# Kernel optimization log

Measured on AMD Instinct MI355X. Metric: run time of the kernel, lower is better.

## Reference

```python
import jax, jax.numpy as jnp
import numpy as np

B, T, P, H, K = 64, 110, 64, 256, 16


def _gru_scan(x_seq, h0, Wih, Whh, bih, bhh):
    """PyTorch-convention GRU. x_seq: (B,L,D), h0: (B,H). Returns (outs (B,L,H), h_last (B,H))."""
    def step(h, x_t):
        gi = x_t @ Wih.T + bih          # (B, 3H)
        gh = h @ Whh.T + bhh            # (B, 3H)
        i_r, i_z, i_n = jnp.split(gi, 3, axis=-1)
        h_r, h_z, h_n = jnp.split(gh, 3, axis=-1)
        r = jax.nn.sigmoid(i_r + h_r)
        zg = jax.nn.sigmoid(i_z + h_z)
        n = jnp.tanh(i_n + r * h_n)
        h_new = (1.0 - zg) * n + zg * h
        return h_new, h_new
    h_last, outs = jax.lax.scan(step, h0, jnp.swapaxes(x_seq, 0, 1))
    return jnp.swapaxes(outs, 0, 1), h_last


def setup_inputs() -> dict:
    key = jax.random.key(0)
    ks = jax.random.split(key, 24)
    s = 0.05
    n = lambda k, shape: (jax.random.normal(k, shape, jnp.float32) * s)
    X = jax.random.normal(ks[0], (B, T, P), jnp.float32)
    # connection: 16 distinct nonzero rows per column, sorted (mimics np.where on a binary mask)
    r = jax.random.uniform(ks[1], (P, P))
    conn_idx = jnp.sort(jnp.argsort(r, axis=0)[:K].T, axis=1).astype(jnp.int32)  # (P, K)
    return dict(
        X=X, conn_idx=conn_idx,
        W_ih_left=n(ks[2], (3 * H, P)), W_hh_left=n(ks[3], (3 * H, H)),
        b_ih_left=n(ks[4], (3 * H,)), b_hh_left=n(ks[5], (3 * H,)),
        W_ih_1=n(ks[6], (3 * H, H)), W_hh_1=n(ks[7], (3 * H, H)),
        b_ih_1=n(ks[8], (3 * H,)), b_hh_1=n(ks[9], (3 * H,)),
        W_mu=n(ks[10], (H, H)), b_mu=n(ks[11], (H,)),
        W_std=n(ks[12], (H, H)), b_std=n(ks[13], (H,)),
        W_mean=n(ks[14], (P, H)), b_mean=n(ks[15], (P,)),
        W_disp=n(ks[16], (P, H)), b_disp=n(ks[17], (P,)),
        W_ih_nets=n(ks[18], (P, 3 * H, K)), W_hh_nets=n(ks[19], (P, 3 * H, H)),
        b_ih_nets=n(ks[20], (P, 3 * H)), b_hh_nets=n(ks[21], (P, 3 * H)),
        W_lin=n(ks[22], (P, 1, H)), b_lin=n(ks[23], (P, 1)),
        z_noise=jax.random.normal(jax.random.fold_in(key, 123), (B, H), jnp.float32),
    )


def reference(X, conn_idx, W_ih_left, W_hh_left, b_ih_left, b_hh_left,
              W_ih_1, W_hh_1, b_ih_1, b_hh_1,
              W_mu, b_mu, W_std, b_std, W_mean, b_mean, W_disp, b_disp,
              W_ih_nets, W_hh_nets, b_ih_nets, b_hh_nets, W_lin, b_lin, z_noise):
    Bb, Tt, Pp = X.shape
    Hh = W_hh_left.shape[1]
    # phase=0, mode='train': prepend a zero timestep
    X_pad = jnp.concatenate([jnp.zeros((Bb, 1, Pp), X.dtype), X], axis=1)  # (B, T+1, P)

    # encoder: gru_left over first 10 real timesteps, h0 = 0
    h0 = jnp.zeros((Bb, Hh), X.dtype)
    _, h_left = _gru_scan(X_pad[:, 1:11, :], h0, W_ih_left, W_hh_left, b_ih_left, b_hh_left)
    # gru_1: single recurrent step with input h_left, hidden 0
    _, h1 = _gru_scan(h_left[:, None, :], h0, W_ih_1, W_hh_1, b_ih_1, b_hh_1)  # (B, H)

    mu = h1 @ W_mu.T + b_mu
    log_var = h1 @ W_std.T + b_std
    mean_ = jnp.clip(jnp.exp(h1 @ W_mean.T + b_mean), 1e-5, 1e6)          # MeanAct
    disp_ = jnp.clip(jax.nn.softplus(h1 @ W_disp.T + b_disp), 1e-4, 1e4)  # DispAct
    z = mu + jnp.exp(0.5 * log_var) * z_noise                             # reparameterize

    # per-series connectivity gather: (B, T+1, P, K) -> (P, B, T+1, K)
    Xg = jnp.transpose(X_pad[:, :, conn_idx], (2, 0, 1, 3))
    # GRU input: cat(X[:, 0:1, :], X[:, 11:-1, :]) -> length L = T - 10
    seq = jnp.concatenate([Xg[:, :, 0:1, :], Xg[:, :, 11:-1, :]], axis=2)  # (P, B, L, K)

    h0_nets = jnp.broadcast_to(z, (Pp, Bb, Hh))
    outs, _ = jax.vmap(_gru_scan, in_axes=(0, 0, 0, 0, 0, 0))(
        seq, h0_nets, W_ih_nets, W_hh_nets, b_ih_nets, b_hh_nets)  # (P, B, L, H)
    outs = jax.nn.relu(outs)
    pred = jnp.einsum('pblh,poh->pblo', outs, W_lin) + b_lin[:, None, None, :]  # (P, B, L, 1)

    return pred, log_var, mu, mean_, disp_
```

## Files before the change

### kernel.cpp

```cpp
#include <hip/hip_runtime.h>


#define OFF_LV   409600
#define OFF_MU   425984
#define OFF_MEAN 442368
#define OFF_DISP 446464

typedef __attribute__((ext_vector_type(8))) short  bf16x8;
typedef __attribute__((ext_vector_type(4))) float  f32x4;

__device__ __forceinline__ float bf2f(unsigned short u) {
    union { unsigned int i; float f; } v; v.i = ((unsigned int)u) << 16; return v.f;
}
__device__ __forceinline__ unsigned short f2bf(float f) {
    union { float f; unsigned int i; } v; v.f = f;
    unsigned int x = v.i;
    return (unsigned short)((x + 0x7FFFu + ((x >> 16) & 1u)) >> 16);
}
__device__ __forceinline__ unsigned short f2bf_fast(float f) {
    return (unsigned short)((__float_as_uint(f) + 0x8000u) >> 16);
}
__device__ __forceinline__ bf16x8 pack8(const float* pf) {
    union { unsigned int u[4]; bf16x8 v; } r;
    const float4 a = *(const float4*)pf;
    const float4 b = *(const float4*)(pf + 4);
    r.u[0] = ((__float_as_uint(a.x) + 0x8000u) >> 16) | ((__float_as_uint(a.y) + 0x8000u) & 0xFFFF0000u);
    r.u[1] = ((__float_as_uint(a.z) + 0x8000u) >> 16) | ((__float_as_uint(a.w) + 0x8000u) & 0xFFFF0000u);
    r.u[2] = ((__float_as_uint(b.x) + 0x8000u) >> 16) | ((__float_as_uint(b.y) + 0x8000u) & 0xFFFF0000u);
    r.u[3] = ((__float_as_uint(b.z) + 0x8000u) >> 16) | ((__float_as_uint(b.w) + 0x8000u) & 0xFFFF0000u);
    return r.v;
}
__device__ __forceinline__ float sigm(float x) {
    return __builtin_amdgcn_rcpf(1.0f + __expf(-x));
}
__device__ __forceinline__ float tanh_fast(float x) {
    return 2.0f * __builtin_amdgcn_rcpf(1.0f + __expf(-2.0f * x)) - 1.0f;
}

#define MFMA(a, b, c) __builtin_amdgcn_mfma_f32_16x16x32_bf16((a), (b), (c), 0, 0, 0)

__global__ __launch_bounds__(512, 1) void encoder_mfma(
    const float* __restrict__ X,
    const float* __restrict__ Wihl_f, const float* __restrict__ Whhl_f,
    const float* __restrict__ bihl,   const float* __restrict__ bhhl,
    const float* __restrict__ Wih1_f, const float* __restrict__ bih1,
    const float* __restrict__ bhh1,
    const float* __restrict__ Wmu_f,  const float* __restrict__ bmu,
    const float* __restrict__ Wstd_f, const float* __restrict__ bstd,
    const float* __restrict__ Wmean_f,const float* __restrict__ bmean,
    const float* __restrict__ Wdisp_f,const float* __restrict__ bdisp,
    float* __restrict__ out)
{
    const int b0   = blockIdx.x * 16;
    const int tid  = threadIdx.x;
    const int wave = tid >> 6;
    const int lane = tid & 63;
    const int quad = lane >> 4;
    const int ncol = lane & 15;
    const int j0   = wave * 32 + ncol;
    const int j1   = j0 + 16;

    __shared__ __align__(16) unsigned short hs[2][16][264];
    __shared__ __align__(16) unsigned short xs[2][16][72];
    __shared__ __align__(16) unsigned short wihl_s[768][72];
    __shared__ float bR[256], bZ[256], bIN[256], bHN[256];
    __shared__ float b1R[256], b1Z[256], b1IN[256], b1HN[256];

    for (int i = tid; i < 768 * 64; i += 512) {
        int row = i >> 6, col = i & 63;
        wihl_s[row][col] = f2bf_fast(Wihl_f[i]);
    }
    for (int i = tid; i < 256; i += 512) {
        bR[i]   = bihl[i]       + bhhl[i];
        bZ[i]   = bihl[256 + i] + bhhl[256 + i];
        bIN[i]  = bihl[512 + i];
        bHN[i]  = bhhl[512 + i];
        b1R[i]  = bih1[i]       + bhh1[i];
        b1Z[i]  = bih1[256 + i] + bhh1[256 + i];
        b1IN[i] = bih1[512 + i];
        b1HN[i] = bhh1[512 + i];
    }
    for (int i = tid; i < 16 * 264; i += 512)
        (&hs[0][0][0])[i] = 0;
    for (int i = tid; i < 1024; i += 512) {
        int b = i >> 6, f = i & 63;
        xs[0][b][f] = f2bf_fast(X[((b0 + b) * 110 + 0) * 64 + f]);
    }

    bf16x8 w_r[2][8], w_z[2][8], w_n[2][8];
    #pragma unroll
    for (int s = 0; s < 2; s++) {
        const int j = s ? j1 : j0;
        #pragma unroll
        for (int k0 = 0; k0 < 8; k0++) {
            const int ko = k0 * 32 + quad * 8;
            w_r[s][k0] = pack8(Whhl_f + (size_t)(j)       * 256 + ko);
            w_z[s][k0] = pack8(Whhl_f + (size_t)(256 + j) * 256 + ko);
            w_n[s][k0] = pack8(Whhl_f + (size_t)(512 + j) * 256 + ko);
        }
    }

    float hreg[2][4];
    #pragma unroll
    for (int s = 0; s < 2; s++)
        #pragma unroll
        for (int r = 0; r < 4; r++) hreg[s][r] = 0.f;

    __syncthreads();

    for (int t = 0; t < 10; t++) {
        const int cur = t & 1, nxt = cur ^ 1;
        f32x4 acc_r[2]  = {{0,0,0,0},{0,0,0,0}};
        f32x4 acc_z[2]  = {{0,0,0,0},{0,0,0,0}};
        f32x4 acc_in[2] = {{0,0,0,0},{0,0,0,0}};
        f32x4 acc_hn[2] = {{0,0,0,0},{0,0,0,0}};

        #pragma unroll
        for (int ks = 0; ks < 2; ks++) {
            const int ko = ks * 32 + quad * 8;
            bf16x8 a = *(const bf16x8*)&xs[cur][ncol][ko];
            #pragma unroll
            for (int s = 0; s < 2; s++) {
                const int j = s ? j1 : j0;
                bf16x8 br = *(const bf16x8*)&wihl_s[j][ko];
                bf16x8 bz = *(const bf16x8*)&wihl_s[256 + j][ko];
                bf16x8 bn = *(const bf16x8*)&wihl_s[512 + j][ko];
                acc_r[s]  = MFMA(a, br, acc_r[s]);
                acc_z[s]  = MFMA(a, bz, acc_z[s]);
                acc_in[s] = MFMA(a, bn, acc_in[s]);
            }
        }
        #pragma unroll
        for (int ks = 0; ks < 8; ks++) {
            bf16x8 a = *(const bf16x8*)&hs[cur][ncol][ks * 32 + quad * 8];
            #pragma unroll
            for (int s = 0; s < 2; s++) {
                acc_r[s]  = MFMA(a, w_r[s][ks], acc_r[s]);
                acc_z[s]  = MFMA(a, w_z[s][ks], acc_z[s]);
                acc_hn[s] = MFMA(a, w_n[s][ks], acc_hn[s]);
            }
        }
        #pragma unroll
        for (int s = 0; s < 2; s++) {
            const int j = s ? j1 : j0;
            #pragma unroll
            for (int r = 0; r < 4; r++) {
                float rg = sigm(acc_r[s][r] + bR[j]);
                float zg = sigm(acc_z[s][r] + bZ[j]);
                float nn = tanh_fast(acc_in[s][r] + bIN[j] + rg * (acc_hn[s][r] + bHN[j]));
                float hv = (1.f - zg) * nn + zg * hreg[s][r];
                hreg[s][r] = hv;
                hs[nxt][quad * 4 + r][j] = f2bf(hv);
            }
        }
        if (t < 9)
            for (int i = tid; i < 1024; i += 512) {
                int b = i >> 6, f = i & 63;
                xs[nxt][b][f] = f2bf_fast(X[((b0 + b) * 110 + (t + 1)) * 64 + f]);
            }
        __syncthreads();
    }

    {
        f32x4 acc_r[2]  = {{0,0,0,0},{0,0,0,0}};
        f32x4 acc_z[2]  = {{0,0,0,0},{0,0,0,0}};
        f32x4 acc_in[2] = {{0,0,0,0},{0,0,0,0}};
        #pragma unroll 2
        for (int ks = 0; ks < 8; ks++) {
            const int ko = ks * 32 + quad * 8;
            bf16x8 a = *(const bf16x8*)&hs[0][ncol][ko];
            #pragma unroll
            for (int s = 0; s < 2; s++) {
                const int j = s ? j1 : j0;
                bf16x8 br = pack8(Wih1_f + (size_t)(j)       * 256 + ko);
                bf16x8 bz = pack8(Wih1_f + (size_t)(256 + j) * 256 + ko);
                bf16x8 bn = pack8(Wih1_f + (size_t)(512 + j) * 256 + ko);
                acc_r[s]  = MFMA(a, br, acc_r[s]);
                acc_z[s]  = MFMA(a, bz, acc_z[s]);
                acc_in[s] = MFMA(a, bn, acc_in[s]);
            }
        }
        #pragma unroll
        for (int s = 0; s < 2; s++) {
            const int j = s ? j1 : j0;
            #pragma unroll
            for (int r = 0; r < 4; r++) {
                float rg = sigm(acc_r[s][r] + b1R[j]);
                float zg = sigm(acc_z[s][r] + b1Z[j]);
                float nn = tanh_fast(acc_in[s][r] + b1IN[j] + rg * b1HN[j]);
                float hv = (1.f - zg) * nn;
                hs[1][quad * 4 + r][j] = f2bf(hv);
            }
        }
        __syncthreads();
    }

    {
        f32x4 acc_mu[2] = {{0,0,0,0},{0,0,0,0}};
        f32x4 acc_lv[2] = {{0,0,0,0},{0,0,0,0}};
        f32x4 acc_md[2] = {{0,0,0,0},{0,0,0,0}};
        const bool do_mean = (wave < 2), do_disp = (wave >= 2 && wave < 4);
        const int jm0 = (wave & 1) * 32 + ncol, jm1 = jm0 + 16;

        #pragma unroll 2
        for (int ks = 0; ks < 8; ks++) {
            const int ko = ks * 32 + quad * 8;
            bf16x8 a = *(const bf16x8*)&hs[1][ncol][ko];
            #pragma unroll
            for (int s = 0; s < 2; s++) {
                const int j = s ? j1 : j0;
                bf16x8 bmu8 = pack8(Wmu_f  + (size_t)j * 256 + ko);
                bf16x8 blv8 = pack8(Wstd_f + (size_t)j * 256 + ko);
                acc_mu[s] = MFMA(a, bmu8, acc_mu[s]);
                acc_lv[s] = MFMA(a, blv8, acc_lv[s]);
                if (do_mean || do_disp) {
                    const int jm = s ? jm1 : jm0;
                    bf16x8 md8 = do_mean ? pack8(Wmean_f + (size_t)jm * 256 + ko)
                                         : pack8(Wdisp_f + (size_t)jm * 256 + ko);
                    acc_md[s] = MFMA(a, md8, acc_md[s]);
                }
            }
        }
        #pragma unroll
        for (int s = 0; s < 2; s++) {
            const int j = s ? j1 : j0;
            const float bmu_v = bmu[j], blv_v = bstd[j];
            #pragma unroll
            for (int r = 0; r < 4; r++) {
                int b = b0 + quad * 4 + r;
                out[OFF_MU + b * 256 + j] = acc_mu[s][r] + bmu_v;
                out[OFF_LV + b * 256 + j] = acc_lv[s][r] + blv_v;
            }
        }
        if (do_mean) {
            #pragma unroll
            for (int s = 0; s < 2; s++) {
                const int jm = s ? jm1 : jm0;
                const float bm = bmean[jm];
                #pragma unroll
                for (int r = 0; r < 4; r++) {
                    int b = b0 + quad * 4 + r;
                    out[OFF_MEAN + b * 64 + jm] =
                        fminf(fmaxf(__expf(acc_md[s][r] + bm), 1e-5f), 1e6f);
                }
            }
        } else if (do_disp) {
            #pragma unroll
            for (int s = 0; s < 2; s++) {
                const int jm = s ? jm1 : jm0;
                const float bd = bdisp[jm];
                #pragma unroll
                for (int r = 0; r < 4; r++) {
                    int b = b0 + quad * 4 + r;
                    float v = acc_md[s][r] + bd;
                    float sp = (v > 20.f) ? v : log1pf(__expf(v));
                    out[OFF_DISP + b * 64 + jm] = fminf(fmaxf(sp, 1e-4f), 1e4f);
                }
            }
        }
    }
}

__global__ __launch_bounds__(512, 2) void nets_kernel(
    const float* __restrict__ X,
    const int*   __restrict__ conn,
    const float* __restrict__ Wih,
    const float* __restrict__ Whh_f,
    const float* __restrict__ bih,
    const float* __restrict__ bhh,
    const float* __restrict__ Wlin,
    const float* __restrict__ blin,
    const float* __restrict__ znoise,
    float*       __restrict__ out)
{
    const int p    = blockIdx.x;
    const int b0   = blockIdx.y * 16;
    const int tid  = threadIdx.x;
    const int wave = tid >> 6;
    const int lane = tid & 63;
    const int quad = lane >> 4;
    const int ncol = lane & 15;
    const int j0   = wave * 32 + ncol;
    const int j1   = j0 + 16;

    __shared__ __align__(16) unsigned short hs[2][16][264];
    __shared__ __align__(16) unsigned short xs[2][16][16];
    __shared__ __align__(16) unsigned short wih_s[768][16];
    __shared__ float bR[256], bZ[256], bIN[256], bHN[256], wlin_s[256];
    __shared__ float predw[2][8][16];
    __shared__ int   conn_s[16];

    for (int i = tid; i < 768 * 16; i += 512)
        (&wih_s[0][0])[i] = f2bf_fast(Wih[p * 768 * 16 + i]);
    for (int i = tid; i < 256; i += 512) {
        bR[i]  = bih[p * 768 + i]       + bhh[p * 768 + i];
        bZ[i]  = bih[p * 768 + 256 + i] + bhh[p * 768 + 256 + i];
        bIN[i] = bih[p * 768 + 512 + i];
        bHN[i] = bhh[p * 768 + 512 + i];
        wlin_s[i] = Wlin[p * 256 + i];
    }
    if (tid < 16) conn_s[tid] = conn[p * 16 + tid];

    for (int i = tid; i < 16 * 264; i += 512) {
        int bb = i / 264, jj = i - bb * 264;
        unsigned short v = 0;
        if (jj < 256) {
            int gi = (b0 + bb) * 256 + jj;
            v = f2bf(out[OFF_MU + gi] + __expf(0.5f * out[OFF_LV + gi]) * znoise[gi]);
        }
        hs[0][bb][jj] = v;
    }
    if (tid < 256) xs[0][tid >> 4][tid & 15] = 0;

    float hreg[2][4];
    #pragma unroll
    for (int s = 0; s < 2; s++)
        #pragma unroll
        for (int r = 0; r < 4; r++) {
            int gi = (b0 + quad * 4 + r) * 256 + (s ? j1 : j0);
            hreg[s][r] = out[OFF_MU + gi] + __expf(0.5f * out[OFF_LV + gi]) * znoise[gi];
        }

    const size_t whh_off = (size_t)p * 768 * 256;
    bf16x8 w_r[2][8], w_z[2][8], w_n[2][8];
    #pragma unroll
    for (int s = 0; s < 2; s++) {
        const int j = s ? j1 : j0;
        #pragma unroll
        for (int k0 = 0; k0 < 8; k0++) {
            const int ko = k0 * 32 + quad * 8;
            w_r[s][k0] = pack8(Whh_f + whh_off + (size_t)(j)       * 256 + ko);
            w_z[s][k0] = pack8(Whh_f + whh_off + (size_t)(256 + j) * 256 + ko);
            w_n[s][k0] = pack8(Whh_f + whh_off + (size_t)(512 + j) * 256 + ko);
        }
    }

    __syncthreads();

    const float blin_v = blin[p];
    const bf16x8 ZERO8 = {0, 0, 0, 0, 0, 0, 0, 0};

    for (int t = 0; t < 100; t++) {
        const int cur = t & 1, nxt = cur ^ 1;
        f32x4 acc_r[2]  = {{0,0,0,0},{0,0,0,0}};
        f32x4 acc_z[2]  = {{0,0,0,0},{0,0,0,0}};
        f32x4 acc_in[2] = {{0,0,0,0},{0,0,0,0}};
        f32x4 acc_hn[2] = {{0,0,0,0},{0,0,0,0}};

        {
            bf16x8 a, br0, bz0, bn0, br1, bz1, bn1;
            if (quad < 2) {
                a   = *(const bf16x8*)&xs[cur][ncol][quad * 8];
                br0 = *(const bf16x8*)&wih_s[j0][quad * 8];
                bz0 = *(const bf16x8*)&wih_s[256 + j0][quad * 8];
                bn0 = *(const bf16x8*)&wih_s[512 + j0][quad * 8];
                br1 = *(const bf16x8*)&wih_s[j1][quad * 8];
                bz1 = *(const bf16x8*)&wih_s[256 + j1][quad * 8];
                bn1 = *(const bf16x8*)&wih_s[512 + j1][quad * 8];
            } else {
                a = ZERO8; br0 = bz0 = bn0 = br1 = bz1 = bn1 = ZERO8;
            }
            acc_r[0]  = MFMA(a, br0, acc_r[0]);  acc_r[1]  = MFMA(a, br1, acc_r[1]);
            acc_z[0]  = MFMA(a, bz0, acc_z[0]);  acc_z[1]  = MFMA(a, bz1, acc_z[1]);
            acc_in[0] = MFMA(a, bn0, acc_in[0]); acc_in[1] = MFMA(a, bn1, acc_in[1]);
        }
        #pragma unroll
        for (int k0 = 0; k0 < 8; k0++) {
            bf16x8 a = *(const bf16x8*)&hs[cur][ncol][k0 * 32 + quad * 8];
            acc_r[0]  = MFMA(a, w_r[0][k0], acc_r[0]);
            acc_r[1]  = MFMA(a, w_r[1][k0], acc_r[1]);
            acc_z[0]  = MFMA(a, w_z[0][k0], acc_z[0]);
            acc_z[1]  = MFMA(a, w_z[1][k0], acc_z[1]);
            acc_hn[0] = MFMA(a, w_n[0][k0], acc_hn[0]);
            acc_hn[1] = MFMA(a, w_n[1][k0], acc_hn[1]);
        }

        float pv[4] = {0.f, 0.f, 0.f, 0.f};
        #pragma unroll
        for (int s = 0; s < 2; s++) {
            const int j = s ? j1 : j0;
            const float b_r = bR[j], b_z = bZ[j], b_in = bIN[j], b_hn = bHN[j];
            const float wl = wlin_s[j];
            #pragma unroll
            for (int r = 0; r < 4; r++) {
                float rg = sigm(acc_r[s][r] + b_r);
                float zg = sigm(acc_z[s][r] + b_z);
                float nn = tanh_fast(acc_in[s][r] + b_in + rg * (acc_hn[s][r] + b_hn));
                float hv = (1.f - zg) * nn + zg * hreg[s][r];
                hreg[s][r] = hv;
                pv[r] += fmaxf(hv, 0.f) * wl;
            }
        }
        #pragma unroll
        for (int r = 0; r < 4; r++) {
            float v = pv[r];
            v += __shfl_xor(v, 1, 64);
            v += __shfl_xor(v, 2, 64);
            v += __shfl_xor(v, 4, 64);
            v += __shfl_xor(v, 8, 64);
            pv[r] = v;
        }

        #pragma unroll
        for (int r = 0; r < 4; r++) {
            hs[nxt][quad * 4 + r][j0] = f2bf_fast(hreg[0][r]);
            hs[nxt][quad * 4 + r][j1] = f2bf_fast(hreg[1][r]);
        }
        if (ncol == 0) {
            #pragma unroll
            for (int r = 0; r < 4; r++)
                predw[cur][wave][quad * 4 + r] = pv[r];
        }
        if (tid < 256) {
            int gb = tid >> 4, gk = tid & 15;
            unsigned short v = 0;
            if (t < 99) v = f2bf_fast(X[(size_t)((b0 + gb) * 110 + (10 + t)) * 64 + conn_s[gk]]);
            xs[nxt][gb][gk] = v;
        }

        __syncthreads();

        if (tid < 16) {
            float s = blin_v;
            #pragma unroll
            for (int w = 0; w < 8; w++) s += predw[cur][w][tid];
            out[(size_t)(p * 64 + b0 + tid) * 100 + t] = s;
        }
    }
}

extern "C" void kernel_launch(void* const* d_in, const int* in_sizes, int n_in,
                              void* d_out, int out_size, void* d_ws, size_t ws_size,
                              hipStream_t stream) {
    const float* X      = (const float*)d_in[0];
    const int*   conn   = (const int*)d_in[1];
    const float* Wihl   = (const float*)d_in[2];
    const float* Whhl   = (const float*)d_in[3];
    const float* bihl   = (const float*)d_in[4];
    const float* bhhl   = (const float*)d_in[5];
    const float* Wih1   = (const float*)d_in[6];
    const float* bih1   = (const float*)d_in[8];
    const float* bhh1   = (const float*)d_in[9];
    const float* Wmu    = (const float*)d_in[10];
    const float* bmu    = (const float*)d_in[11];
    const float* Wstd   = (const float*)d_in[12];
    const float* bstd   = (const float*)d_in[13];
    const float* Wmean  = (const float*)d_in[14];
    const float* bmean  = (const float*)d_in[15];
    const float* Wdisp  = (const float*)d_in[16];
    const float* bdisp  = (const float*)d_in[17];
    const float* Wihn   = (const float*)d_in[18];
    const float* Whhn   = (const float*)d_in[19];
    const float* bihn   = (const float*)d_in[20];
    const float* bhhn   = (const float*)d_in[21];
    const float* Wlin   = (const float*)d_in[22];
    const float* blin   = (const float*)d_in[23];
    const float* znoise = (const float*)d_in[24];

    float* out = (float*)d_out;
    (void)d_ws; (void)ws_size;

    encoder_mfma<<<4, 512, 0, stream>>>(
        X, Wihl, Whhl, bihl, bhhl, Wih1, bih1, bhh1,
        Wmu, bmu, Wstd, bstd, Wmean, bmean, Wdisp, bdisp, out);

    nets_kernel<<<dim3(64, 4), 512, 0, stream>>>(
        X, conn, Wihn, Whhn, bihn, bhhn, Wlin, blin, znoise, out);
}
```

Before: 528.6 us.

## Fuse encoder GRU into per-series nets kernel, recomputing encoder redundantly per block

Merges the two launches into one kernel. Each of the 256 blocks recomputes the 10-step encoder GRU, the gru_1 step and the mu/logvar heads for its 16-sample batch slice. The block then seeds its per-series GRU directly from the reparameterized z kept in registers and LDS, instead of reading mu and log_var back from global memory. This removes the second kernel launch and the serial dependency on a 4-block encoder kernel, at the cost of 64x redundant encoder work. The encoder input weights are now read from global memory (cache) rather than staged in LDS, to keep shared memory small enough for two blocks per CU.

```diff
diff --git a/kernel.cpp b/kernel.cpp
--- a/kernel.cpp
+++ b/kernel.cpp
@@ -39,8 +39,9 @@
 
 #define MFMA(a, b, c) __builtin_amdgcn_mfma_f32_16x16x32_bf16((a), (b), (c), 0, 0, 0)
 
-__global__ __launch_bounds__(512, 1) void encoder_mfma(
+__global__ __launch_bounds__(512, 2) void granger_fused(
     const float* __restrict__ X,
+    const int*   __restrict__ conn,
     const float* __restrict__ Wihl_f, const float* __restrict__ Whhl_f,
     const float* __restrict__ bihl,   const float* __restrict__ bhhl,
     const float* __restrict__ Wih1_f, const float* __restrict__ bih1,
@@ -49,227 +50,9 @@
     const float* __restrict__ Wstd_f, const float* __restrict__ bstd,
     const float* __restrict__ Wmean_f,const float* __restrict__ bmean,
     const float* __restrict__ Wdisp_f,const float* __restrict__ bdisp,
-    float* __restrict__ out)
-{
-    const int b0   = blockIdx.x * 16;
-    const int tid  = threadIdx.x;
-    const int wave = tid >> 6;
-    const int lane = tid & 63;
-    const int quad = lane >> 4;
-    const int ncol = lane & 15;
-    const int j0   = wave * 32 + ncol;
-    const int j1   = j0 + 16;
-
-    __shared__ __align__(16) unsigned short hs[2][16][264];
-    __shared__ __align__(16) unsigned short xs[2][16][72];
-    __shared__ __align__(16) unsigned short wihl_s[768][72];
-    __shared__ float bR[256], bZ[256], bIN[256], bHN[256];
-    __shared__ float b1R[256], b1Z[256], b1IN[256], b1HN[256];
-
-    for (int i = tid; i < 768 * 64; i += 512) {
-        int row = i >> 6, col = i & 63;
-        wihl_s[row][col] = f2bf_fast(Wihl_f[i]);
-    }
-    for (int i = tid; i < 256; i += 512) {
-        bR[i]   = bihl[i]       + bhhl[i];
-        bZ[i]   = bihl[256 + i] + bhhl[256 + i];
-        bIN[i]  = bihl[512 + i];
-        bHN[i]  = bhhl[512 + i];
-        b1R[i]  = bih1[i]       + bhh1[i];
-        b1Z[i]  = bih1[256 + i] + bhh1[256 + i];
-        b1IN[i] = bih1[512 + i];
-        b1HN[i] = bhh1[512 + i];
-    }
-    for (int i = tid; i < 16 * 264; i += 512)
-        (&hs[0][0][0])[i] = 0;
-    for (int i = tid; i < 1024; i += 512) {
-        int b = i >> 6, f = i & 63;
-        xs[0][b][f] = f2bf_fast(X[((b0 + b) * 110 + 0) * 64 + f]);
-    }
-
-    bf16x8 w_r[2][8], w_z[2][8], w_n[2][8];
-    #pragma unroll
-    for (int s = 0; s < 2; s++) {
-        const int j = s ? j1 : j0;
-        #pragma unroll
-        for (int k0 = 0; k0 < 8; k0++) {
-            const int ko = k0 * 32 + quad * 8;
-            w_r[s][k0] = pack8(Whhl_f + (size_t)(j)       * 256 + ko);
-            w_z[s][k0] = pack8(Whhl_f + (size_t)(256 + j) * 256 + ko);
-            w_n[s][k0] = pack8(Whhl_f + (size_t)(512 + j) * 256 + ko);
-        }
-    }
-
-    float hreg[2][4];
-    #pragma unroll
-    for (int s = 0; s < 2; s++)
-        #pragma unroll
-        for (int r = 0; r < 4; r++) hreg[s][r] = 0.f;
-
-    __syncthreads();
-
-    for (int t = 0; t < 10; t++) {
-        const int cur = t & 1, nxt = cur ^ 1;
-        f32x4 acc_r[2]  = {{0,0,0,0},{0,0,0,0}};
-        f32x4 acc_z[2]  = {{0,0,0,0},{0,0,0,0}};
-        f32x4 acc_in[2] = {{0,0,0,0},{0,0,0,0}};
-        f32x4 acc_hn[2] = {{0,0,0,0},{0,0,0,0}};
-
-        #pragma unroll
-        for (int ks = 0; ks < 2; ks++) {
-            const int ko = ks * 32 + quad * 8;
-            bf16x8 a = *(const bf16x8*)&xs[cur][ncol][ko];
-            #pragma unroll
-            for (int s = 0; s < 2; s++) {
-                const int j = s ? j1 : j0;
-                bf16x8 br = *(const bf16x8*)&wihl_s[j][ko];
-                bf16x8 bz = *(const bf16x8*)&wihl_s[256 + j][ko];
-                bf16x8 bn = *(const bf16x8*)&wihl_s[512 + j][ko];
-                acc_r[s]  = MFMA(a, br, acc_r[s]);
-                acc_z[s]  = MFMA(a, bz, acc_z[s]);
-                acc_in[s] = MFMA(a, bn, acc_in[s]);
-            }
-        }
-        #pragma unroll
-        for (int ks = 0; ks < 8; ks++) {
-            bf16x8 a = *(const bf16x8*)&hs[cur][ncol][ks * 32 + quad * 8];
-            #pragma unroll
-            for (int s = 0; s < 2; s++) {
-                acc_r[s]  = MFMA(a, w_r[s][ks], acc_r[s]);
-                acc_z[s]  = MFMA(a, w_z[s][ks], acc_z[s]);
-                acc_hn[s] = MFMA(a, w_n[s][ks], acc_hn[s]);
-            }
-        }
-        #pragma unroll
-        for (int s = 0; s < 2; s++) {
-            const int j = s ? j1 : j0;
-            #pragma unroll
-            for (int r = 0; r < 4; r++) {
-                float rg = sigm(acc_r[s][r] + bR[j]);
-                float zg = sigm(acc_z[s][r] + bZ[j]);
-                float nn = tanh_fast(acc_in[s][r] + bIN[j] + rg * (acc_hn[s][r] + bHN[j]));
-                float hv = (1.f - zg) * nn + zg * hreg[s][r];
-                hreg[s][r] = hv;
-                hs[nxt][quad * 4 + r][j] = f2bf(hv);
-            }
-        }
-        if (t < 9)
-            for (int i = tid; i < 1024; i += 512) {
-                int b = i >> 6, f = i & 63;
-                xs[nxt][b][f] = f2bf_fast(X[((b0 + b) * 110 + (t + 1)) * 64 + f]);
-            }
-        __syncthreads();
-    }
-
-    {
-        f32x4 acc_r[2]  = {{0,0,0,0},{0,0,0,0}};
-        f32x4 acc_z[2]  = {{0,0,0,0},{0,0,0,0}};
-        f32x4 acc_in[2] = {{0,0,0,0},{0,0,0,0}};
-        #pragma unroll 2
-        for (int ks = 0; ks < 8; ks++) {
-            const int ko = ks * 32 + quad * 8;
-            bf16x8 a = *(const bf16x8*)&hs[0][ncol][ko];
-            #pragma unroll
-            for (int s = 0; s < 2; s++) {
-                const int j = s ? j1 : j0;
-                bf16x8 br = pack8(Wih1_f + (size_t)(j)       * 256 + ko);
-                bf16x8 bz = pack8(Wih1_f + (size_t)(256 + j) * 256 + ko);
-                bf16x8 bn = pack8(Wih1_f + (size_t)(512 + j) * 256 + ko);
-                acc_r[s]  = MFMA(a, br, acc_r[s]);
-                acc_z[s]  = MFMA(a, bz, acc_z[s]);
-                acc_in[s] = MFMA(a, bn, acc_in[s]);
-            }
-        }
-        #pragma unroll
-        for (int s = 0; s < 2; s++) {
-            const int j = s ? j1 : j0;
-            #pragma unroll
-            for (int r = 0; r < 4; r++) {
-                float rg = sigm(acc_r[s][r] + b1R[j]);
-                float zg = sigm(acc_z[s][r] + b1Z[j]);
-                float nn = tanh_fast(acc_in[s][r] + b1IN[j] + rg * b1HN[j]);
-                float hv = (1.f - zg) * nn;
-                hs[1][quad * 4 + r][j] = f2bf(hv);
-            }
-        }
-        __syncthreads();
-    }
-
-    {
-        f32x4 acc_mu[2] = {{0,0,0,0},{0,0,0,0}};
-        f32x4 acc_lv[2] = {{0,0,0,0},{0,0,0,0}};
-        f32x4 acc_md[2] = {{0,0,0,0},{0,0,0,0}};
-        const bool do_mean = (wave < 2), do_disp = (wave >= 2 && wave < 4);
-        const int jm0 = (wave & 1) * 32 + ncol, jm1 = jm0 + 16;
-
-        #pragma unroll 2
-        for (int ks = 0; ks < 8; ks++) {
-            const int ko = ks * 32 + quad * 8;
-            bf16x8 a = *(const bf16x8*)&hs[1][ncol][ko];
-            #pragma unroll
-            for (int s = 0; s < 2; s++) {
-                const int j = s ? j1 : j0;
-                bf16x8 bmu8 = pack8(Wmu_f  + (size_t)j * 256 + ko);
-                bf16x8 blv8 = pack8(Wstd_f + (size_t)j * 256 + ko);
-                acc_mu[s] = MFMA(a, bmu8, acc_mu[s]);
-                acc_lv[s] = MFMA(a, blv8, acc_lv[s]);
-                if (do_mean || do_disp) {
-                    const int jm = s ? jm1 : jm0;
-                    bf16x8 md8 = do_mean ? pack8(Wmean_f + (size_t)jm * 256 + ko)
-                                         : pack8(Wdisp_f + (size_t)jm * 256 + ko);
-                    acc_md[s] = MFMA(a, md8, acc_md[s]);
-                }
-            }
-        }
-        #pragma unroll
-        for (int s = 0; s < 2; s++) {
-            const int j = s ? j1 : j0;
-            const float bmu_v = bmu[j], blv_v = bstd[j];
-            #pragma unroll
-            for (int r = 0; r < 4; r++) {
-                int b = b0 + quad * 4 + r;
-                out[OFF_MU + b * 256 + j] = acc_mu[s][r] + bmu_v;
-                out[OFF_LV + b * 256 + j] = acc_lv[s][r] + blv_v;
-            }
-        }
-        if (do_mean) {
-            #pragma unroll
-            for (int s = 0; s < 2; s++) {
-                const int jm = s ? jm1 : jm0;
-                const float bm = bmean[jm];
-                #pragma unroll
-                for (int r = 0; r < 4; r++) {
-                    int b = b0 + quad * 4 + r;
-                    out[OFF_MEAN + b * 64 + jm] =
-                        fminf(fmaxf(__expf(acc_md[s][r] + bm), 1e-5f), 1e6f);
-                }
-            }
-        } else if (do_disp) {
-            #pragma unroll
-            for (int s = 0; s < 2; s++) {
-                const int jm = s ? jm1 : jm0;
-                const float bd = bdisp[jm];
-                #pragma unroll
-                for (int r = 0; r < 4; r++) {
-                    int b = b0 + quad * 4 + r;
-                    float v = acc_md[s][r] + bd;
-                    float sp = (v > 20.f) ? v : log1pf(__expf(v));
-                    out[OFF_DISP + b * 64 + jm] = fminf(fmaxf(sp, 1e-4f), 1e4f);
-                }
-            }
-        }
-    }
-}
-
-__global__ __launch_bounds__(512, 2) void nets_kernel(
-    const float* __restrict__ X,
-    const int*   __restrict__ conn,
-    const float* __restrict__ Wih,
-    const float* __restrict__ Whh_f,
-    const float* __restrict__ bih,
-    const float* __restrict__ bhh,
-    const float* __restrict__ Wlin,
-    const float* __restrict__ blin,
+    const float* __restrict__ Wih,    const float* __restrict__ Whh_f,
+    const float* __restrict__ bih,    const float* __restrict__ bhh,
+    const float* __restrict__ Wlin,   const float* __restrict__ blin,
     const float* __restrict__ znoise,
     float*       __restrict__ out)
 {
@@ -284,11 +67,216 @@
     const int j1   = j0 + 16;
 
     __shared__ __align__(16) unsigned short hs[2][16][264];
-    __shared__ __align__(16) unsigned short xs[2][16][16];
+    __shared__ __align__(16) unsigned short xse[2][16][72];
+    __shared__ __align__(16) unsigned short xsn[2][16][16];
     __shared__ __align__(16) unsigned short wih_s[768][16];
-    __shared__ float bR[256], bZ[256], bIN[256], bHN[256], wlin_s[256];
+    __shared__ float bR[256], bZ[256], bIN[256], bHN[256];
+    __shared__ float b1R[256], b1Z[256], b1IN[256], b1HN[256];
+    __shared__ float wlin_s[256];
     __shared__ float predw[2][8][16];
     __shared__ int   conn_s[16];
+
+    for (int i = tid; i < 256; i += 512) {
+        bR[i]   = bihl[i]       + bhhl[i];
+        bZ[i]   = bihl[256 + i] + bhhl[256 + i];
+        bIN[i]  = bihl[512 + i];
+        bHN[i]  = bhhl[512 + i];
+        b1R[i]  = bih1[i]       + bhh1[i];
+        b1Z[i]  = bih1[256 + i] + bhh1[256 + i];
+        b1IN[i] = bih1[512 + i];
+        b1HN[i] = bhh1[512 + i];
+    }
+    for (int i = tid; i < 16 * 264; i += 512)
+        (&hs[0][0][0])[i] = 0;
+    for (int i = tid; i < 1024; i += 512) {
+        int b = i >> 6, f = i & 63;
+        xse[0][b][f] = f2bf_fast(X[((b0 + b) * 110 + 0) * 64 + f]);
+    }
+
+    bf16x8 w_r[2][8], w_z[2][8], w_n[2][8];
+    #pragma unroll
+    for (int s = 0; s < 2; s++) {
+        const int j = s ? j1 : j0;
+        #pragma unroll
+        for (int k0 = 0; k0 < 8; k0++) {
+            const int ko = k0 * 32 + quad * 8;
+            w_r[s][k0] = pack8(Whhl_f + (size_t)(j)       * 256 + ko);
+            w_z[s][k0] = pack8(Whhl_f + (size_t)(256 + j) * 256 + ko);
+            w_n[s][k0] = pack8(Whhl_f + (size_t)(512 + j) * 256 + ko);
+        }
+    }
+
+    float hreg[2][4];
+    #pragma unroll
+    for (int s = 0; s < 2; s++)
+        #pragma unroll
+        for (int r = 0; r < 4; r++) hreg[s][r] = 0.f;
+
+    __syncthreads();
+
+    const float* wxl = Wihl_f;
+    for (int t = 0; t < 10; t++) {
+        asm("" : "+v"(wxl));
+        const int cur = t & 1, nxt = cur ^ 1;
+        f32x4 acc_r[2]  = {{0,0,0,0},{0,0,0,0}};
+        f32x4 acc_z[2]  = {{0,0,0,0},{0,0,0,0}};
+        f32x4 acc_in[2] = {{0,0,0,0},{0,0,0,0}};
+        f32x4 acc_hn[2] = {{0,0,0,0},{0,0,0,0}};
+
+        #pragma unroll
+        for (int ks = 0; ks < 2; ks++) {
+            const int ko = ks * 32 + quad * 8;
+            bf16x8 a = *(const bf16x8*)&xse[cur][ncol][ko];
+            #pragma unroll
+            for (int s = 0; s < 2; s++) {
+                const int j = s ? j1 : j0;
+                bf16x8 br = pack8(wxl + (size_t)(j)       * 64 + ko);
+                bf16x8 bz = pack8(wxl + (size_t)(256 + j) * 64 + ko);
+                bf16x8 bn = pack8(wxl + (size_t)(512 + j) * 64 + ko);
+                acc_r[s]  = MFMA(a, br, acc_r[s]);
+                acc_z[s]  = MFMA(a, bz, acc_z[s]);
+                acc_in[s] = MFMA(a, bn, acc_in[s]);
+            }
+        }
+        #pragma unroll
+        for (int ks = 0; ks < 8; ks++) {
+            bf16x8 a = *(const bf16x8*)&hs[cur][ncol][ks * 32 + quad * 8];
+            #pragma unroll
+            for (int s = 0; s < 2; s++) {
+                acc_r[s]  = MFMA(a, w_r[s][ks], acc_r[s]);
+                acc_z[s]  = MFMA(a, w_z[s][ks], acc_z[s]);
+                acc_hn[s] = MFMA(a, w_n[s][ks], acc_hn[s]);
+            }
+        }
+        #pragma unroll
+        for (int s = 0; s < 2; s++) {
+            const int j = s ? j1 : j0;
+            #pragma unroll
+            for (int r = 0; r < 4; r++) {
+                float rg = sigm(acc_r[s][r] + bR[j]);
+                float zg = sigm(acc_z[s][r] + bZ[j]);
+                float nn = tanh_fast(acc_in[s][r] + bIN[j] + rg * (acc_hn[s][r] + bHN[j]));
+                float hv = (1.f - zg) * nn + zg * hreg[s][r];
+                hreg[s][r] = hv;
+                hs[nxt][quad * 4 + r][j] = f2bf(hv);
+            }
+        }
+        if (t < 9)
+            for (int i = tid; i < 1024; i += 512) {
+                int b = i >> 6, f = i & 63;
+                xse[nxt][b][f] = f2bf_fast(X[((b0 + b) * 110 + (t + 1)) * 64 + f]);
+            }
+        __syncthreads();
+    }
+
+    {
+        f32x4 acc_r[2]  = {{0,0,0,0},{0,0,0,0}};
+        f32x4 acc_z[2]  = {{0,0,0,0},{0,0,0,0}};
+        f32x4 acc_in[2] = {{0,0,0,0},{0,0,0,0}};
+        #pragma unroll 2
+        for (int ks = 0; ks < 8; ks++) {
+            const int ko = ks * 32 + quad * 8;
+            bf16x8 a = *(const bf16x8*)&hs[0][ncol][ko];
+            #pragma unroll
+            for (int s = 0; s < 2; s++) {
+                const int j = s ? j1 : j0;
+                bf16x8 br = pack8(Wih1_f + (size_t)(j)       * 256 + ko);
+                bf16x8 bz = pack8(Wih1_f + (size_t)(256 + j) * 256 + ko);
+                bf16x8 bn = pack8(Wih1_f + (size_t)(512 + j) * 256 + ko);
+                acc_r[s]  = MFMA(a, br, acc_r[s]);
+                acc_z[s]  = MFMA(a, bz, acc_z[s]);
+                acc_in[s] = MFMA(a, bn, acc_in[s]);
+            }
+        }
+        #pragma unroll
+        for (int s = 0; s < 2; s++) {
+            const int j = s ? j1 : j0;
+            #pragma unroll
+            for (int r = 0; r < 4; r++) {
+                float rg = sigm(acc_r[s][r] + b1R[j]);
+                float zg = sigm(acc_z[s][r] + b1Z[j]);
+                float nn = tanh_fast(acc_in[s][r] + b1IN[j] + rg * b1HN[j]);
+                float hv = (1.f - zg) * nn;
+                hs[1][quad * 4 + r][j] = f2bf(hv);
+            }
+        }
+        __syncthreads();
+    }
+
+    {
+        f32x4 acc_mu[2] = {{0,0,0,0},{0,0,0,0}};
+        f32x4 acc_lv[2] = {{0,0,0,0},{0,0,0,0}};
+        f32x4 acc_md[2] = {{0,0,0,0},{0,0,0,0}};
+        const bool headp   = (p == 0);
+        const bool do_mean = headp && (wave < 2);
+        const bool do_disp = headp && (wave >= 2 && wave < 4);
+        const int jm0 = (wave & 1) * 32 + ncol, jm1 = jm0 + 16;
+
+        #pragma unroll 2
+        for (int ks = 0; ks < 8; ks++) {
+            const int ko = ks * 32 + quad * 8;
+            bf16x8 a = *(const bf16x8*)&hs[1][ncol][ko];
+            #pragma unroll
+            for (int s = 0; s < 2; s++) {
+                const int j = s ? j1 : j0;
+                bf16x8 bmu8 = pack8(Wmu_f  + (size_t)j * 256 + ko);
+                bf16x8 blv8 = pack8(Wstd_f + (size_t)j * 256 + ko);
+                acc_mu[s] = MFMA(a, bmu8, acc_mu[s]);
+                acc_lv[s] = MFMA(a, blv8, acc_lv[s]);
+                if (do_mean || do_disp) {
+                    const int jm = s ? jm1 : jm0;
+                    bf16x8 md8 = do_mean ? pack8(Wmean_f + (size_t)jm * 256 + ko)
+                                         : pack8(Wdisp_f + (size_t)jm * 256 + ko);
+                    acc_md[s] = MFMA(a, md8, acc_md[s]);
+                }
+            }
+        }
+        #pragma unroll
+        for (int s = 0; s < 2; s++) {
+            const int j = s ? j1 : j0;
+            const float bmu_v = bmu[j], blv_v = bstd[j];
+            #pragma unroll
+            for (int r = 0; r < 4; r++) {
+                const int row = quad * 4 + r, b = b0 + row;
+                float muv = acc_mu[s][r] + bmu_v;
+                float lvv = acc_lv[s][r] + blv_v;
+                if (headp) {
+                    out[OFF_MU + b * 256 + j] = muv;
+                    out[OFF_LV + b * 256 + j] = lvv;
+                }
+                float zv = muv + __expf(0.5f * lvv) * znoise[b * 256 + j];
+                hreg[s][r] = zv;
+                hs[0][row][j] = f2bf(zv);
+            }
+        }
+        if (do_mean) {
+            #pragma unroll
+            for (int s = 0; s < 2; s++) {
+                const int jm = s ? jm1 : jm0;
+                const float bm = bmean[jm];
+                #pragma unroll
+                for (int r = 0; r < 4; r++) {
+                    int b = b0 + quad * 4 + r;
+                    out[OFF_MEAN + b * 64 + jm] =
+                        fminf(fmaxf(__expf(acc_md[s][r] + bm), 1e-5f), 1e6f);
+                }
+            }
+        } else if (do_disp) {
+            #pragma unroll
+            for (int s = 0; s < 2; s++) {
+                const int jm = s ? jm1 : jm0;
+                const float bd = bdisp[jm];
+                #pragma unroll
+                for (int r = 0; r < 4; r++) {
+                    int b = b0 + quad * 4 + r;
+                    float v = acc_md[s][r] + bd;
+                    float sp = (v > 20.f) ? v : log1pf(__expf(v));
+                    out[OFF_DISP + b * 64 + jm] = fminf(fmaxf(sp, 1e-4f), 1e4f);
+                }
+            }
+        }
+    }
+    __syncthreads();
 
     for (int i = tid; i < 768 * 16; i += 512)
         (&wih_s[0][0])[i] = f2bf_fast(Wih[p * 768 * 16 + i]);
@@ -300,29 +288,9 @@
         wlin_s[i] = Wlin[p * 256 + i];
     }
     if (tid < 16) conn_s[tid] = conn[p * 16 + tid];
-
-    for (int i = tid; i < 16 * 264; i += 512) {
-        int bb = i / 264, jj = i - bb * 264;
-        unsigned short v = 0;
-        if (jj < 256) {
-            int gi = (b0 + bb) * 256 + jj;
-            v = f2bf(out[OFF_MU + gi] + __expf(0.5f * out[OFF_LV + gi]) * znoise[gi]);
-        }
-        hs[0][bb][jj] = v;
-    }
-    if (tid < 256) xs[0][tid >> 4][tid & 15] = 0;
-
-    float hreg[2][4];
-    #pragma unroll
-    for (int s = 0; s < 2; s++)
-        #pragma unroll
-        for (int r = 0; r < 4; r++) {
-            int gi = (b0 + quad * 4 + r) * 256 + (s ? j1 : j0);
-            hreg[s][r] = out[OFF_MU + gi] + __expf(0.5f * out[OFF_LV + gi]) * znoise[gi];
-        }
+    if (tid < 256) xsn[0][tid >> 4][tid & 15] = 0;
 
     const size_t whh_off = (size_t)p * 768 * 256;
-    bf16x8 w_r[2][8], w_z[2][8], w_n[2][8];
     #pragma unroll
     for (int s = 0; s < 2; s++) {
         const int j = s ? j1 : j0;
@@ -350,7 +318,7 @@
         {
             bf16x8 a, br0, bz0, bn0, br1, bz1, bn1;
             if (quad < 2) {
-                a   = *(const bf16x8*)&xs[cur][ncol][quad * 8];
+                a   = *(const bf16x8*)&xsn[cur][ncol][quad * 8];
                 br0 = *(const bf16x8*)&wih_s[j0][quad * 8];
                 bz0 = *(const bf16x8*)&wih_s[256 + j0][quad * 8];
                 bn0 = *(const bf16x8*)&wih_s[512 + j0][quad * 8];
@@ -415,7 +383,7 @@
             int gb = tid >> 4, gk = tid & 15;
             unsigned short v = 0;
             if (t < 99) v = f2bf_fast(X[(size_t)((b0 + gb) * 110 + (10 + t)) * 64 + conn_s[gk]]);
-            xs[nxt][gb][gk] = v;
+            xsn[nxt][gb][gk] = v;
         }
 
         __syncthreads();
@@ -460,10 +428,8 @@
     float* out = (float*)d_out;
     (void)d_ws; (void)ws_size;
 
-    encoder_mfma<<<4, 512, 0, stream>>>(
-        X, Wihl, Whhl, bihl, bhhl, Wih1, bih1, bhh1,
-        Wmu, bmu, Wstd, bstd, Wmean, bmean, Wdisp, bdisp, out);
-
-    nets_kernel<<<dim3(64, 4), 512, 0, stream>>>(
-        X, conn, Wihn, Whhn, bihn, bhhn, Wlin, blin, znoise, out);
-}
+    granger_fused<<<dim3(64, 4), 512, 0, stream>>>(
+        X, conn, Wihl, Whhl, bihl, bhhl, Wih1, bih1, bhh1,
+        Wmu, bmu, Wstd, bstd, Wmean, bmean, Wdisp, bdisp,
+        Wihn, Whhn, bihn, bhhn, Wlin, blin, znoise, out);
+}
```

New measurement: 582.4 us. 10.2% more time.

## Move latent heads from encoder into nets kernel with redundant per-block recompute

Applied to the files above, without the earlier changes.

The encoder kernel now stops after the GRU and writes h1 as bf16 to workspace. The mu/log_var/mean/disp projections and the reparameterization move into the nets kernel: every block recomputes mu and log_var for its 16 batch rows and seeds its hidden state directly. Only the p==0 blocks write the head outputs. This takes the head GEMMs off the 4-block encoder's serial path, at the cost of each of the 256 nets blocks re-reading the Wmu/Wstd weights and doing redundant MFMA work.

```diff
diff --git a/kernel.cpp b/kernel.cpp
--- a/kernel.cpp
+++ b/kernel.cpp
@@ -39,17 +39,13 @@
 
 #define MFMA(a, b, c) __builtin_amdgcn_mfma_f32_16x16x32_bf16((a), (b), (c), 0, 0, 0)
 
-__global__ __launch_bounds__(512, 1) void encoder_mfma(
+__global__ __launch_bounds__(512, 1) void encoder_core(
     const float* __restrict__ X,
     const float* __restrict__ Wihl_f, const float* __restrict__ Whhl_f,
     const float* __restrict__ bihl,   const float* __restrict__ bhhl,
     const float* __restrict__ Wih1_f, const float* __restrict__ bih1,
     const float* __restrict__ bhh1,
-    const float* __restrict__ Wmu_f,  const float* __restrict__ bmu,
-    const float* __restrict__ Wstd_f, const float* __restrict__ bstd,
-    const float* __restrict__ Wmean_f,const float* __restrict__ bmean,
-    const float* __restrict__ Wdisp_f,const float* __restrict__ bdisp,
-    float* __restrict__ out)
+    unsigned short* __restrict__ h1out)
 {
     const int b0   = blockIdx.x * 16;
     const int tid  = threadIdx.x;
@@ -195,17 +191,73 @@
         __syncthreads();
     }
 
+    for (int i = tid; i < 16 * 256; i += 512) {
+        int row = i >> 8, j = i & 255;
+        h1out[(size_t)(b0 + row) * 256 + j] = hs[1][row][j];
+    }
+}
+
+__global__ __launch_bounds__(512, 2) void nets_kernel(
+    const float* __restrict__ X,
+    const int*   __restrict__ conn,
+    const float* __restrict__ Wih,
+    const float* __restrict__ Whh_f,
+    const float* __restrict__ bih,
+    const float* __restrict__ bhh,
+    const float* __restrict__ Wlin,
+    const float* __restrict__ blin,
+    const float* __restrict__ znoise,
+    const unsigned short* __restrict__ h1g,
+    const float* __restrict__ Wmu_f,  const float* __restrict__ bmu,
+    const float* __restrict__ Wstd_f, const float* __restrict__ bstd,
+    const float* __restrict__ Wmean_f,const float* __restrict__ bmean,
+    const float* __restrict__ Wdisp_f,const float* __restrict__ bdisp,
+    float*       __restrict__ out)
+{
+    const int p    = blockIdx.x;
+    const int b0   = blockIdx.y * 16;
+    const int tid  = threadIdx.x;
+    const int wave = tid >> 6;
+    const int lane = tid & 63;
+    const int quad = lane >> 4;
+    const int ncol = lane & 15;
+    const int j0   = wave * 32 + ncol;
+    const int j1   = j0 + 16;
+
+    __shared__ __align__(16) unsigned short hs[2][16][264];
+    __shared__ __align__(16) unsigned short xs[2][16][16];
+    __shared__ __align__(16) unsigned short wih_s[768][16];
+    __shared__ float bR[256], bZ[256], bIN[256], bHN[256], wlin_s[256];
+    __shared__ float predw[2][8][16];
+    __shared__ int   conn_s[16];
+
+    for (int i = tid; i < 768 * 16; i += 512)
+        (&wih_s[0][0])[i] = f2bf_fast(Wih[p * 768 * 16 + i]);
+    for (int i = tid; i < 256; i += 512) {
+        bR[i]  = bih[p * 768 + i]       + bhh[p * 768 + i];
+        bZ[i]  = bih[p * 768 + 256 + i] + bhh[p * 768 + 256 + i];
+        bIN[i] = bih[p * 768 + 512 + i];
+        bHN[i] = bhh[p * 768 + 512 + i];
+        wlin_s[i] = Wlin[p * 256 + i];
+    }
+    if (tid < 16) conn_s[tid] = conn[p * 16 + tid];
+    if (tid < 256) xs[0][tid >> 4][tid & 15] = 0;
+
+    float hreg[2][4];
+
     {
         f32x4 acc_mu[2] = {{0,0,0,0},{0,0,0,0}};
         f32x4 acc_lv[2] = {{0,0,0,0},{0,0,0,0}};
         f32x4 acc_md[2] = {{0,0,0,0},{0,0,0,0}};
-        const bool do_mean = (wave < 2), do_disp = (wave >= 2 && wave < 4);
+        const bool headp   = (p == 0);
+        const bool do_mean = headp && (wave < 2);
+        const bool do_disp = headp && (wave >= 2 && wave < 4);
         const int jm0 = (wave & 1) * 32 + ncol, jm1 = jm0 + 16;
 
         #pragma unroll 2
         for (int ks = 0; ks < 8; ks++) {
             const int ko = ks * 32 + quad * 8;
-            bf16x8 a = *(const bf16x8*)&hs[1][ncol][ko];
+            bf16x8 a = *(const bf16x8*)&h1g[(size_t)(b0 + ncol) * 256 + ko];
             #pragma unroll
             for (int s = 0; s < 2; s++) {
                 const int j = s ? j1 : j0;
@@ -227,9 +279,16 @@
             const float bmu_v = bmu[j], blv_v = bstd[j];
             #pragma unroll
             for (int r = 0; r < 4; r++) {
-                int b = b0 + quad * 4 + r;
-                out[OFF_MU + b * 256 + j] = acc_mu[s][r] + bmu_v;
-                out[OFF_LV + b * 256 + j] = acc_lv[s][r] + blv_v;
+                const int row = quad * 4 + r, b = b0 + row;
+                float muv = acc_mu[s][r] + bmu_v;
+                float lvv = acc_lv[s][r] + blv_v;
+                if (headp) {
+                    out[OFF_MU + b * 256 + j] = muv;
+                    out[OFF_LV + b * 256 + j] = lvv;
+                }
+                float zv = muv + __expf(0.5f * lvv) * znoise[b * 256 + j];
+                hreg[s][r] = zv;
+                hs[0][row][j] = f2bf(zv);
             }
         }
         if (do_mean) {
@@ -259,67 +318,6 @@
             }
         }
     }
-}
-
-__global__ __launch_bounds__(512, 2) void nets_kernel(
-    const float* __restrict__ X,
-    const int*   __restrict__ conn,
-    const float* __restrict__ Wih,
-    const float* __restrict__ Whh_f,
-    const float* __restrict__ bih,
-    const float* __restrict__ bhh,
-    const float* __restrict__ Wlin,
-    const float* __restrict__ blin,
-    const float* __restrict__ znoise,
-    float*       __restrict__ out)
-{
-    const int p    = blockIdx.x;
-    const int b0   = blockIdx.y * 16;
-    const int tid  = threadIdx.x;
-    const int wave = tid >> 6;
-    const int lane = tid & 63;
-    const int quad = lane >> 4;
-    const int ncol = lane & 15;
-    const int j0   = wave * 32 + ncol;
-    const int j1   = j0 + 16;
-
-    __shared__ __align__(16) unsigned short hs[2][16][264];
-    __shared__ __align__(16) unsigned short xs[2][16][16];
-    __shared__ __align__(16) unsigned short wih_s[768][16];
-    __shared__ float bR[256], bZ[256], bIN[256], bHN[256], wlin_s[256];
-    __shared__ float predw[2][8][16];
-    __shared__ int   conn_s[16];
-
-    for (int i = tid; i < 768 * 16; i += 512)
-        (&wih_s[0][0])[i] = f2bf_fast(Wih[p * 768 * 16 + i]);
-    for (int i = tid; i < 256; i += 512) {
-        bR[i]  = bih[p * 768 + i]       + bhh[p * 768 + i];
-        bZ[i]  = bih[p * 768 + 256 + i] + bhh[p * 768 + 256 + i];
-        bIN[i] = bih[p * 768 + 512 + i];
-        bHN[i] = bhh[p * 768 + 512 + i];
-        wlin_s[i] = Wlin[p * 256 + i];
-    }
-    if (tid < 16) conn_s[tid] = conn[p * 16 + tid];
-
-    for (int i = tid; i < 16 * 264; i += 512) {
-        int bb = i / 264, jj = i - bb * 264;
-        unsigned short v = 0;
-        if (jj < 256) {
-            int gi = (b0 + bb) * 256 + jj;
-            v = f2bf(out[OFF_MU + gi] + __expf(0.5f * out[OFF_LV + gi]) * znoise[gi]);
-        }
-        hs[0][bb][jj] = v;
-    }
-    if (tid < 256) xs[0][tid >> 4][tid & 15] = 0;
-
-    float hreg[2][4];
-    #pragma unroll
-    for (int s = 0; s < 2; s++)
-        #pragma unroll
-        for (int r = 0; r < 4; r++) {
-            int gi = (b0 + quad * 4 + r) * 256 + (s ? j1 : j0);
-            hreg[s][r] = out[OFF_MU + gi] + __expf(0.5f * out[OFF_LV + gi]) * znoise[gi];
-        }
 
     const size_t whh_off = (size_t)p * 768 * 256;
     bf16x8 w_r[2][8], w_z[2][8], w_n[2][8];
@@ -458,12 +456,13 @@
     const float* znoise = (const float*)d_in[24];
 
     float* out = (float*)d_out;
-    (void)d_ws; (void)ws_size;
-
-    encoder_mfma<<<4, 512, 0, stream>>>(
-        X, Wihl, Whhl, bihl, bhhl, Wih1, bih1, bhh1,
-        Wmu, bmu, Wstd, bstd, Wmean, bmean, Wdisp, bdisp, out);
+    unsigned short* h1ws = (unsigned short*)d_ws;
+    (void)ws_size;
+
+    encoder_core<<<4, 512, 0, stream>>>(
+        X, Wihl, Whhl, bihl, bhhl, Wih1, bih1, bhh1, h1ws);
 
     nets_kernel<<<dim3(64, 4), 512, 0, stream>>>(
-        X, conn, Wihn, Whhn, bihn, bhhn, Wlin, blin, znoise, out);
-}
+        X, conn, Wihn, Whhn, bihn, bhhn, Wlin, blin, znoise,
+        h1ws, Wmu, bmu, Wstd, bstd, Wmean, bmean, Wdisp, bdisp, out);
+}
```

After: 518.1 us. 2.0% less time.
